# Optimization experiments

Hardware: AMD Instinct MI355X
Metric: run time of the kernel (lower is better)

Reference implementation:

```python
import jax, jax.numpy as jnp
import numpy as np

N = 20000      # num nodes
E = 320000     # num edges
F_IN = 512
HEADS = 8
D = 64         # out_features per head (512 / 8)
ALPHA = 0.2    # leaky relu slope
EPS = 1e-16


def setup_inputs() -> dict:
    key = jax.random.key(0)
    k1, k2, k3, k4, k5 = jax.random.split(key, 5)
    x = jax.random.normal(k1, (N, F_IN), dtype=jnp.float32)
    edge_index = jax.random.randint(k2, (2, E), 0, N, dtype=jnp.int64)
    # per-head parameters (xavier-normal-ish scale)
    s_w = np.sqrt(2.0 / (F_IN + D))
    W_e = jax.random.normal(k3, (HEADS, F_IN, D), dtype=jnp.float32) * s_w
    W_r = jax.random.normal(k4, (HEADS, F_IN, D), dtype=jnp.float32) * s_w
    # attention vector over concat of [h_src, h_dst, diff, |diff|, prod] -> 5*D
    s_a = np.sqrt(2.0 / (1 + 5 * D))
    a = jax.random.normal(k5, (HEADS, 5 * D), dtype=jnp.float32) * s_a
    return {"x": x, "edge_index": edge_index, "W_e": W_e, "W_r": W_r, "a": a}


def _gat_forward(x, edge_index, W_e, W_r, a):
    src = edge_index[0]  # [E] softmax / output rows
    dst = edge_index[1]  # [E]

    h_e = jnp.einsum('nf,hfd->hnd', x, W_e)  # [H,N,D]
    h_r = jnp.einsum('nf,hfd->hnd', x, W_r)  # [H,N,D]

    a_src, a_dst, a_dif, a_abs, a_prd = jnp.split(a, 5, axis=1)  # each [H,D]

    # node-level dot products for the linear concat parts, then gather
    s_src = jnp.einsum('hnd,hd->hn', h_e, a_src)[:, src]  # [H,E]
    s_dst = jnp.einsum('hnd,hd->hn', h_e, a_dst)[:, dst]  # [H,E]

    hr_src = h_r[:, src]            # [H,E,D]
    hr_dst = h_r[:, dst]            # [H,E,D]
    diff = hr_dst - hr_src          # [H,E,D]
    score = (s_src + s_dst
             + jnp.einsum('hed,hd->he', diff, a_dif)
             + jnp.einsum('hed,hd->he', jnp.abs(diff), a_abs)
             + jnp.einsum('hed,hd->he', hr_src * hr_dst, a_prd))  # [H,E]

    alpha = jax.nn.leaky_relu(score, negative_slope=ALPHA)  # [H,E]

    # sparse softmax over edges grouped by source node
    alpha_t = alpha.T  # [E,H]
    m = jax.ops.segment_max(alpha_t, src, num_segments=N)        # [N,H]
    ex = jnp.exp(alpha_t - m[src])                                # [E,H]
    denom = jax.ops.segment_sum(ex, src, num_segments=N)[src]    # [E,H]
    att = ex / (denom + EPS)                                      # [E,H]

    # spmm: out[src] += att * h_e[dst]
    msg = att[:, :, None] * jnp.transpose(h_e[:, dst], (1, 0, 2))  # [E,H,D]
    out = jax.ops.segment_sum(msg, src, num_segments=N)            # [N,H,D]
    return out.reshape(N, HEADS * D)  # concat heads along feature dim


def reference(x, edge_index, W_e, W_r, a):
    return _gat_forward(x, edge_index, W_e, W_r, a)
```

## Files before the change

### kernel.cpp

```cpp
#include <hip/hip_runtime.h>
#include <hip/hip_bf16.h>

#define N_NODES 20000
#define N_EDGES 320000
#define F_IN 512
#define HEADS 8
#define DH 64
#define KPAD 64

typedef _Float16 f16;
typedef __attribute__((ext_vector_type(8))) _Float16 half8;
typedef __attribute__((ext_vector_type(4))) _Float16 half4v;
typedef __attribute__((ext_vector_type(2))) _Float16 half2v;
typedef __attribute__((ext_vector_type(4))) float f32x4;

__device__ __forceinline__ void async_copy16(void* lds_base, const void* g) {
  __builtin_amdgcn_global_load_lds(
      (const __attribute__((address_space(1))) unsigned int*)g,
      (__attribute__((address_space(3))) unsigned int*)lds_base, 16, 0, 0);
}

#define CX_BLOCKS 2500
#define CW_BLOCKS 128
#define SCAT_BLOCKS 1250

__global__ __launch_bounds__(256) void prologue_kernel(
    const float* __restrict__ x, const float* __restrict__ We,
    const float* __restrict__ Wr, const int* __restrict__ ei,
    f16* __restrict__ xh, f16* __restrict__ Wt,
    int* __restrict__ cnt, int* __restrict__ csr)
{
  __shared__ f16 tile[64 * 65];
  const int b = blockIdx.x;
  if (b < CX_BLOCKS) {
    int base = (b * 256 + threadIdx.x) * 4;
    #pragma unroll
    for (int rep = 0; rep < 4; ++rep) {
      int i = base + rep * (CX_BLOCKS * 256 * 4);
      float4 v = *(const float4*)&x[i];
      half4v o;
      o[0] = (f16)v.x; o[1] = (f16)v.y; o[2] = (f16)v.z; o[3] = (f16)v.w;
      *(half4v*)&xh[i] = o;
    }
  } else if (b < CX_BLOCKS + CW_BLOCKS) {
    const int bb = b - CX_BLOCKS;
    const int kt = (bb & 7) * 64;
    const int h = (bb >> 3) & 7;
    const int mat = bb >> 6;
    const float* __restrict__ W = (mat ? Wr : We) + (size_t)h * F_IN * DH;
    #pragma unroll
    for (int r = 0; r < 16; ++r) {
      int idx = r * 256 + threadIdx.x;
      int k = idx >> 6, d = idx & 63;
      tile[d * 65 + k] = (f16)W[(size_t)(kt + k) * DH + d];
    }
    __syncthreads();
    f16* __restrict__ Wo = Wt + (size_t)(mat * 8 + h) * 64 * F_IN;
    #pragma unroll
    for (int r = 0; r < 16; ++r) {
      int idx = r * 256 + threadIdx.x;
      int d = idx >> 6, k = idx & 63;
      Wo[(size_t)d * F_IN + kt + k] = tile[d * 65 + k];
    }
  } else {
    int e = (b - CX_BLOCKS - CW_BLOCKS) * 256 + threadIdx.x;
    if (e < N_EDGES) {
      int s = ei[e];
      int t = ei[N_EDGES + e];
      int pos = atomicAdd(&cnt[s], 1);
      if (pos < KPAD) csr[s * KPAD + pos] = t;
    }
  }
}

#define GBM 128
#define GBN 128
#define GBK 64
#define MT_TOTAL 157
#define MT_PER_GRP 20
#define NKT (F_IN / GBK)
#define TSTR 72

__global__ __launch_bounds__(256) void gemm_mfma(
    const f16* __restrict__ xh, const f16* __restrict__ Wt,
    f16* __restrict__ hef, const float* __restrict__ a,
    float* __restrict__ ssrc, float* __restrict__ sdst)
{
  const int b = blockIdx.x;
  const int g = b & 7;
  const int j = b >> 3;
  const int m_tile = g * MT_PER_GRP + (j >> 3);
  const int c_tile = j & 7;
  if (m_tile >= MT_TOTAL) return;

  __shared__ f16 smem[32768];
  f16* __restrict__ As = smem;
  f16* __restrict__ Bs = smem + 16384;
  const int tid = threadIdx.x;
  const int m0 = m_tile * GBM;
  const int n0 = c_tile * GBN;
  const int wv = tid >> 6, lane = tid & 63, quad = lane >> 4, l16 = lane & 15;
  const int wm = (wv >> 1) * 64;
  const int wn = (wv & 1) * 64;
  const int lrow = lane >> 3;
  const int gc = (lane & 7) ^ (lrow & 7);

  f32x4 acc[4][4] = {};

  auto stage = [&](int kt, int buf) {
    #pragma unroll
    for (int s = 0; s < 4; ++s) {
      int seg = wv * 4 + s;
      int row = seg * 8 + lrow;
      async_copy16(&As[buf * 8192 + seg * 512],
                   &xh[(size_t)(m0 + row) * F_IN + kt + gc * 8]);
      async_copy16(&Bs[buf * 8192 + seg * 512],
                   &Wt[(size_t)(n0 + row) * F_IN + kt + gc * 8]);
    }
  };

  stage(0, 0);
  __syncthreads();
  for (int it = 0; it < NKT; ++it) {
    if (it + 1 < NKT) stage((it + 1) * GBK, (it + 1) & 1);
    const f16* __restrict__ Ab = &As[(it & 1) * 8192];
    const f16* __restrict__ Bb = &Bs[(it & 1) * 8192];
    #pragma unroll
    for (int ks = 0; ks < 2; ++ks) {
      half8 af[4], bf4[4];
      const int ch = ((ks << 2) + quad) ^ (l16 & 7);
      #pragma unroll
      for (int i = 0; i < 4; ++i)
        af[i] = *(const half8*)&Ab[(wm + i * 16 + l16) * GBK + ch * 8];
      #pragma unroll
      for (int jj = 0; jj < 4; ++jj)
        bf4[jj] = *(const half8*)&Bb[(wn + jj * 16 + l16) * GBK + ch * 8];
      #pragma unroll
      for (int i = 0; i < 4; ++i)
        #pragma unroll
        for (int jj = 0; jj < 4; ++jj)
          acc[i][jj] = __builtin_amdgcn_mfma_f32_16x16x32_f16(af[i], bf4[jj], acc[i][jj], 0, 0, 0);
    }
    __syncthreads();
  }

  const int cb = c_tile * 2 + (wv & 1);
  const int mat = cb >> 3, h = cb & 7;

  {
    f16* __restrict__ tb = smem + wv * (64 * TSTR);
    #pragma unroll
    for (int i = 0; i < 4; ++i)
      #pragma unroll
      for (int jj = 0; jj < 4; ++jj)
        #pragma unroll
        for (int r = 0; r < 4; ++r)
          tb[(i * 16 + quad * 4 + r) * TSTR + jj * 16 + l16] = (f16)acc[i][jj][r];
    const int rrow = lane >> 3;
    const int rseg = lane & 7;
    #pragma unroll
    for (int g2 = 0; g2 < 8; ++g2) {
      int row = g2 * 8 + rrow;
      half8 vv = *(const half8*)&tb[row * TSTR + rseg * 8];
      int m = m0 + wm + row;
      if (m < N_NODES)
        *(half8*)&hef[(size_t)m * 1024 + mat * 512 + h * DH + rseg * 8] = vv;
    }
  }

  if (mat == 0) {
    float as4[4], ad4[4];
    #pragma unroll
    for (int jj = 0; jj < 4; ++jj) {
      as4[jj] = a[h * 320 + jj * 16 + l16];
      ad4[jj] = a[h * 320 + 64 + jj * 16 + l16];
    }
    #pragma unroll
    for (int i = 0; i < 4; ++i) {
      #pragma unroll
      for (int r = 0; r < 4; ++r) {
        int m = m0 + wm + i * 16 + quad * 4 + r;
        float v1 = 0.f, v2 = 0.f;
        #pragma unroll
        for (int jj = 0; jj < 4; ++jj) {
          v1 = fmaf(acc[i][jj][r], as4[jj], v1);
          v2 = fmaf(acc[i][jj][r], ad4[jj], v2);
        }
        #pragma unroll
        for (int s = 1; s < 16; s <<= 1) {
          v1 += __shfl_xor(v1, s);
          v2 += __shfl_xor(v2, s);
        }
        if (l16 == 0 && m < N_NODES) {
          ssrc[(size_t)m * HEADS + h] = v1;
          sdst[(size_t)m * HEADS + h] = v2;
        }
      }
    }
  }
}

__global__ __launch_bounds__(256) void attn_kernel(
    const f16* __restrict__ hef, const float* __restrict__ a,
    const float* __restrict__ ssrc, const float* __restrict__ sdst,
    const int* __restrict__ cnt, const int* __restrict__ csr,
    float* __restrict__ out)
{
  const int wv = threadIdx.x >> 6;
  const int n = blockIdx.x * 4 + wv;
  const int lane = threadIdx.x & 63;
  const int h = lane >> 3;
  const int d0 = (lane & 7) * 8;
  const int deg = min(cnt[n], KPAD);
  const int beg = n * KPAD, end = beg + deg;

  const half8 hrn = *(const half8*)&hef[(size_t)n * 1024 + lane * 8 + 512];
  half2v adif2[4], aabs2[4], aprd2[4];
  const int ab = h * 320;
  #pragma unroll
  for (int c = 0; c < 4; ++c) {
    adif2[c][0] = (f16)a[ab + 128 + d0 + 2 * c];
    adif2[c][1] = (f16)a[ab + 128 + d0 + 2 * c + 1];
    aabs2[c][0] = (f16)a[ab + 192 + d0 + 2 * c];
    aabs2[c][1] = (f16)a[ab + 192 + d0 + 2 * c + 1];
    aprd2[c][0] = (f16)a[ab + 256 + d0 + 2 * c];
    aprd2[c][1] = (f16)a[ab + 256 + d0 + 2 * c + 1];
  }
  const float sbase = ssrc[(size_t)n * HEADS + h];

  float denom = 0.f;
  float acc[8] = {};

  auto edge = [&](half8 he8, half8 hr8, float sd) {
    half8 df = hr8 - hrn;
    uint4 u = __builtin_bit_cast(uint4, df);
    u.x &= 0x7FFF7FFFu; u.y &= 0x7FFF7FFFu; u.z &= 0x7FFF7FFFu; u.w &= 0x7FFF7FFFu;
    half8 ad = __builtin_bit_cast(half8, u);
    half8 pr = hr8 * hrn;
    float v = 0.f;
    #pragma unroll
    for (int c = 0; c < 4; ++c) {
      half2v df2 = {df[2 * c], df[2 * c + 1]};
      half2v ad2 = {ad[2 * c], ad[2 * c + 1]};
      half2v pr2 = {pr[2 * c], pr[2 * c + 1]};
      v = __builtin_amdgcn_fdot2(df2, adif2[c], v, false);
      v = __builtin_amdgcn_fdot2(ad2, aabs2[c], v, false);
      v = __builtin_amdgcn_fdot2(pr2, aprd2[c], v, false);
    }
    v += __shfl_xor(v, 1);
    v += __shfl_xor(v, 2);
    v += __shfl_xor(v, 4);
    float sc = sbase + sd + v;
    sc = fmaxf(sc, 0.2f * sc);
    float ex = __expf(sc);
    denom += ex;
    #pragma unroll
    for (int jj = 0; jj < 8; ++jj) acc[jj] = fmaf(ex, (float)he8[jj], acc[jj]);
  };

  int i = beg;
  for (; i + 2 <= end; i += 2) {
    int t0 = csr[i], t1 = csr[i + 1];
    size_t b0 = (size_t)t0 * 1024 + lane * 8;
    size_t b1 = (size_t)t1 * 1024 + lane * 8;
    half8 e0 = *(const half8*)&hef[b0];
    half8 r0 = *(const half8*)&hef[b0 + 512];
    half8 e1 = *(const half8*)&hef[b1];
    half8 r1 = *(const half8*)&hef[b1 + 512];
    float s0 = sdst[(size_t)t0 * HEADS + h];
    float s1 = sdst[(size_t)t1 * HEADS + h];
    edge(e0, r0, s0);
    edge(e1, r1, s1);
  }
  if (i < end) {
    int t = csr[i];
    size_t b0 = (size_t)t * 1024 + lane * 8;
    half8 e0 = *(const half8*)&hef[b0];
    half8 r0 = *(const half8*)&hef[b0 + 512];
    edge(e0, r0, sdst[(size_t)t * HEADS + h]);
  }

  float inv = 1.f / (denom + 1e-16f);
  float4 o0, o1;
  o0.x = acc[0] * inv; o0.y = acc[1] * inv; o0.z = acc[2] * inv; o0.w = acc[3] * inv;
  o1.x = acc[4] * inv; o1.y = acc[5] * inv; o1.z = acc[6] * inv; o1.w = acc[7] * inv;
  *(float4*)&out[(size_t)n * 512 + lane * 8] = o0;
  *(float4*)&out[(size_t)n * 512 + lane * 8 + 4] = o1;
}

extern "C" void kernel_launch(void* const* d_in, const int* in_sizes, int n_in,
                              void* d_out, int out_size, void* d_ws, size_t ws_size,
                              hipStream_t stream) {
  const float* x  = (const float*)d_in[0];
  const int*   ei = (const int*)d_in[1];
  const float* We = (const float*)d_in[2];
  const float* Wr = (const float*)d_in[3];
  const float* a  = (const float*)d_in[4];
  float* out = (float*)d_out;

  char* ws = (char*)d_ws;
  size_t p = 0;
  auto alloc = [&](size_t bytes) {
    void* r = ws + p;
    p = (p + bytes + 255) & ~(size_t)255;
    return r;
  };
  f16* xh  = (f16*)alloc(sizeof(f16) * (size_t)N_NODES * F_IN);
  f16* Wt  = (f16*)alloc(sizeof(f16) * 2 * HEADS * F_IN * DH);
  f16* hef = (f16*)alloc(sizeof(f16) * (size_t)N_NODES * 1024);
  float* ssrc = (float*)alloc(sizeof(float) * (size_t)N_NODES * HEADS);
  float* sdst = (float*)alloc(sizeof(float) * (size_t)N_NODES * HEADS);
  int* cnt = (int*)alloc(sizeof(int) * N_NODES);
  int* csr = (int*)alloc(sizeof(int) * (size_t)N_NODES * KPAD);

  hipMemsetAsync(cnt, 0, sizeof(int) * N_NODES, stream);

  prologue_kernel<<<CX_BLOCKS + CW_BLOCKS + SCAT_BLOCKS, 256, 0, stream>>>(
      x, We, Wr, ei, xh, Wt, cnt, csr);

  gemm_mfma<<<8 * MT_PER_GRP * 8, 256, 0, stream>>>(xh, Wt, hef, a, ssrc, sdst);

  attn_kernel<<<N_NODES / 4, 256, 0, stream>>>(hef, a, ssrc, sdst, cnt, csr, out);
}
```

Before: 251.1 us.

## Fold linear attention terms into extra GEMM columns via precomputed weight projections

Precomputes per-head projected weight vectors (W_e·a_src − W_r·a_dif and W_e·a_dst + W_r·a_dif) in the prologue and appends them as 16 extra output columns of the GEMM. The node scores ssrc/sdst, which now also carry the linear diff term, come straight out of the MFMA accumulator instead of a shuffle reduction. The per-edge diff dot product in the attention kernel is dropped. This adds a ninth column tile per M-tile, most of which is wasted (only 16 of 128 columns used), and rounds the projected weights to fp16.

```diff
diff --git a/kernel.cpp b/kernel.cpp
--- a/kernel.cpp
+++ b/kernel.cpp
@@ -22,11 +22,13 @@
 
 #define CX_BLOCKS 2500
 #define CW_BLOCKS 128
+#define WA_BLOCKS 16
 #define SCAT_BLOCKS 1250
 
 __global__ __launch_bounds__(256) void prologue_kernel(
     const float* __restrict__ x, const float* __restrict__ We,
-    const float* __restrict__ Wr, const int* __restrict__ ei,
+    const float* __restrict__ Wr, const float* __restrict__ a,
+    const int* __restrict__ ei,
     f16* __restrict__ xh, f16* __restrict__ Wt,
     int* __restrict__ cnt, int* __restrict__ csr)
 {
@@ -62,8 +64,25 @@
       int d = idx >> 6, k = idx & 63;
       Wo[(size_t)d * F_IN + kt + k] = tile[d * 65 + k];
     }
+  } else if (b < CX_BLOCKS + CW_BLOCKS + WA_BLOCKS) {
+    const int j = b - CX_BLOCKS - CW_BLOCKS;
+    const int h = j & 7, sel = j >> 3;
+    const float* __restrict__ ae = a + h * 320 + (sel ? 64 : 0);
+    const float* __restrict__ ad = a + h * 320 + 128;
+    const float sgn = sel ? 1.f : -1.f;
+    #pragma unroll
+    for (int rep = 0; rep < 2; ++rep) {
+      int k = rep * 256 + threadIdx.x;
+      const float* __restrict__ we = We + ((size_t)h * F_IN + k) * DH;
+      const float* __restrict__ wr = Wr + ((size_t)h * F_IN + k) * DH;
+      float s = 0.f;
+      #pragma unroll
+      for (int d = 0; d < DH; ++d)
+        s = fmaf(we[d], ae[d], fmaf(sgn * wr[d], ad[d], s));
+      Wt[(size_t)(1024 + j) * F_IN + k] = (f16)s;
+    }
   } else {
-    int e = (b - CX_BLOCKS - CW_BLOCKS) * 256 + threadIdx.x;
+    int e = (b - CX_BLOCKS - CW_BLOCKS - WA_BLOCKS) * 256 + threadIdx.x;
     if (e < N_EDGES) {
       int s = ei[e];
       int t = ei[N_EDGES + e];
@@ -78,19 +97,21 @@
 #define GBK 64
 #define MT_TOTAL 157
 #define MT_PER_GRP 20
+#define NCT 9
 #define NKT (F_IN / GBK)
 #define TSTR 72
 
 __global__ __launch_bounds__(256) void gemm_mfma(
     const f16* __restrict__ xh, const f16* __restrict__ Wt,
-    f16* __restrict__ hef, const float* __restrict__ a,
+    f16* __restrict__ hef,
     float* __restrict__ ssrc, float* __restrict__ sdst)
 {
   const int b = blockIdx.x;
   const int g = b & 7;
   const int j = b >> 3;
-  const int m_tile = g * MT_PER_GRP + (j >> 3);
-  const int c_tile = j & 7;
+  const int mg = j / NCT;
+  const int m_tile = g * MT_PER_GRP + mg;
+  const int c_tile = j - mg * NCT;
   if (m_tile >= MT_TOTAL) return;
 
   __shared__ f16 smem[32768];
@@ -147,7 +168,7 @@
   const int cb = c_tile * 2 + (wv & 1);
   const int mat = cb >> 3, h = cb & 7;
 
-  {
+  if (mat < 2) {
     f16* __restrict__ tb = smem + wv * (64 * TSTR);
     #pragma unroll
     for (int i = 0; i < 4; ++i)
@@ -166,34 +187,16 @@
       if (m < N_NODES)
         *(half8*)&hef[(size_t)m * 1024 + mat * 512 + h * DH + rseg * 8] = vv;
     }
-  }
-
-  if (mat == 0) {
-    float as4[4], ad4[4];
-    #pragma unroll
-    for (int jj = 0; jj < 4; ++jj) {
-      as4[jj] = a[h * 320 + jj * 16 + l16];
-      ad4[jj] = a[h * 320 + 64 + jj * 16 + l16];
-    }
+  } else if (cb == 16) {
     #pragma unroll
     for (int i = 0; i < 4; ++i) {
       #pragma unroll
       for (int r = 0; r < 4; ++r) {
         int m = m0 + wm + i * 16 + quad * 4 + r;
-        float v1 = 0.f, v2 = 0.f;
-        #pragma unroll
-        for (int jj = 0; jj < 4; ++jj) {
-          v1 = fmaf(acc[i][jj][r], as4[jj], v1);
-          v2 = fmaf(acc[i][jj][r], ad4[jj], v2);
-        }
-        #pragma unroll
-        for (int s = 1; s < 16; s <<= 1) {
-          v1 += __shfl_xor(v1, s);
-          v2 += __shfl_xor(v2, s);
-        }
-        if (l16 == 0 && m < N_NODES) {
-          ssrc[(size_t)m * HEADS + h] = v1;
-          sdst[(size_t)m * HEADS + h] = v2;
+        if (m < N_NODES) {
+          float v = acc[i][0][r];
+          if (l16 < 8) ssrc[(size_t)m * HEADS + l16] = v;
+          else         sdst[(size_t)m * HEADS + (l16 - 8)] = v;
         }
       }
     }
@@ -215,12 +218,10 @@
   const int beg = n * KPAD, end = beg + deg;
 
   const half8 hrn = *(const half8*)&hef[(size_t)n * 1024 + lane * 8 + 512];
-  half2v adif2[4], aabs2[4], aprd2[4];
+  half2v aabs2[4], aprd2[4];
   const int ab = h * 320;
   #pragma unroll
   for (int c = 0; c < 4; ++c) {
-    adif2[c][0] = (f16)a[ab + 128 + d0 + 2 * c];
-    adif2[c][1] = (f16)a[ab + 128 + d0 + 2 * c + 1];
     aabs2[c][0] = (f16)a[ab + 192 + d0 + 2 * c];
     aabs2[c][1] = (f16)a[ab + 192 + d0 + 2 * c + 1];
     aprd2[c][0] = (f16)a[ab + 256 + d0 + 2 * c];
@@ -237,16 +238,15 @@
     u.x &= 0x7FFF7FFFu; u.y &= 0x7FFF7FFFu; u.z &= 0x7FFF7FFFu; u.w &= 0x7FFF7FFFu;
     half8 ad = __builtin_bit_cast(half8, u);
     half8 pr = hr8 * hrn;
-    float v = 0.f;
+    float va = 0.f, vb = 0.f;
     #pragma unroll
     for (int c = 0; c < 4; ++c) {
-      half2v df2 = {df[2 * c], df[2 * c + 1]};
       half2v ad2 = {ad[2 * c], ad[2 * c + 1]};
       half2v pr2 = {pr[2 * c], pr[2 * c + 1]};
-      v = __builtin_amdgcn_fdot2(df2, adif2[c], v, false);
-      v = __builtin_amdgcn_fdot2(ad2, aabs2[c], v, false);
-      v = __builtin_amdgcn_fdot2(pr2, aprd2[c], v, false);
-    }
+      va = __builtin_amdgcn_fdot2(ad2, aabs2[c], va, false);
+      vb = __builtin_amdgcn_fdot2(pr2, aprd2[c], vb, false);
+    }
+    float v = va + vb;
     v += __shfl_xor(v, 1);
     v += __shfl_xor(v, 2);
     v += __shfl_xor(v, 4);
@@ -306,7 +306,7 @@
     return r;
   };
   f16* xh  = (f16*)alloc(sizeof(f16) * (size_t)N_NODES * F_IN);
-  f16* Wt  = (f16*)alloc(sizeof(f16) * 2 * HEADS * F_IN * DH);
+  f16* Wt  = (f16*)alloc(sizeof(f16) * (size_t)1152 * F_IN);
   f16* hef = (f16*)alloc(sizeof(f16) * (size_t)N_NODES * 1024);
   float* ssrc = (float*)alloc(sizeof(float) * (size_t)N_NODES * HEADS);
   float* sdst = (float*)alloc(sizeof(float) * (size_t)N_NODES * HEADS);
@@ -315,10 +315,10 @@
 
   hipMemsetAsync(cnt, 0, sizeof(int) * N_NODES, stream);
 
-  prologue_kernel<<<CX_BLOCKS + CW_BLOCKS + SCAT_BLOCKS, 256, 0, stream>>>(
-      x, We, Wr, ei, xh, Wt, cnt, csr);
-
-  gemm_mfma<<<8 * MT_PER_GRP * 8, 256, 0, stream>>>(xh, Wt, hef, a, ssrc, sdst);
+  prologue_kernel<<<CX_BLOCKS + CW_BLOCKS + WA_BLOCKS + SCAT_BLOCKS, 256, 0, stream>>>(
+      x, We, Wr, a, ei, xh, Wt, cnt, csr);
+
+  gemm_mfma<<<8 * MT_PER_GRP * NCT, 256, 0, stream>>>(xh, Wt, hef, ssrc, sdst);
 
   attn_kernel<<<N_NODES / 4, 256, 0, stream>>>(hef, a, ssrc, sdst, cnt, csr, out);
 }
```

New measurement: 241.5 us. -3.8%, faster.
